# Optimization experiments

Measured on AMD Instinct MI355X. Metric: run time of the kernel, lower is better.

## Reference

```python
import jax, jax.numpy as jnp
import numpy as np

H = 64  # hidden size

def _lstm_forward(x, W_ih, W_hh, b_ih, b_hh):
    # x: [B, T, 1]; PyTorch gate order: i, f, g, o
    B = x.shape[0]
    # precompute input contribution for all timesteps: [B, T, 4H]
    x_gates = jnp.einsum('bti,gi->btg', x, W_ih) + b_ih + b_hh

    def step(carry, xg):
        h, c = carry                      # [B, H] each
        gates = xg + h @ W_hh.T           # [B, 4H]
        i = jax.nn.sigmoid(gates[:, 0*H:1*H])
        f = jax.nn.sigmoid(gates[:, 1*H:2*H])
        g = jnp.tanh(gates[:, 2*H:3*H])
        o = jax.nn.sigmoid(gates[:, 3*H:4*H])
        c_new = f * c + i * g
        h_new = o * jnp.tanh(c_new)
        return (h_new, c_new), None

    h0 = jnp.zeros((B, H), dtype=x.dtype)
    c0 = jnp.zeros((B, H), dtype=x.dtype)
    (h_last, _), _ = jax.lax.scan(step, (h0, c0), jnp.swapaxes(x_gates, 0, 1))
    return h_last

def setup_inputs() -> dict:
    key = jax.random.key(0)
    ks = jax.random.split(key, 7)
    B, T = 262144, 5
    s = 1.0 / np.sqrt(H)  # pytorch LSTM default init scale
    return {
        'x':    jax.random.normal(ks[0], (B, T, 1), dtype=jnp.float32),
        'W_ih': jax.random.uniform(ks[1], (4*H, 1), jnp.float32, -s, s),
        'W_hh': jax.random.uniform(ks[2], (4*H, H), jnp.float32, -s, s),
        'b_ih': jax.random.uniform(ks[3], (4*H,), jnp.float32, -s, s),
        'b_hh': jax.random.uniform(ks[4], (4*H,), jnp.float32, -s, s),
        'W_fc': jax.random.uniform(ks[5], (1, H), jnp.float32, -s, s),
        'b_fc': jax.random.uniform(ks[6], (1,), jnp.float32, -s, s),
    }

def reference(x, W_ih, W_hh, b_ih, b_hh, W_fc, b_fc):
    h_last = _lstm_forward(x, W_ih, W_hh, b_ih, b_hh)  # [B, H]
    return h_last @ W_fc.T + b_fc                      # [B, 1]
```

## Files before the change

### kernel.cpp

```cpp
#include <hip/hip_runtime.h>

#define HDIM   64
#define TSTEPS 5
#define WAVES  8
#define BLOCK  (WAVES * 64)
#define EPW    16
#define EPB    (WAVES * EPW)

typedef _Float16 f16x8 __attribute__((ext_vector_type(8)));
typedef float    f32x4 __attribute__((ext_vector_type(4)));

#define L2E 1.44269504088896340736f

__device__ __forceinline__ float rcp_(float x) { return __builtin_amdgcn_rcpf(x); }
__device__ __forceinline__ float ex2_(float x) { return __builtin_amdgcn_exp2f(x); }
__device__ __forceinline__ float sigp_(float v) { return rcp_(1.0f + ex2_(-v)); }

__global__ __launch_bounds__(BLOCK, 4) void lstm_mfma_kernel(
    const float* __restrict__ x,
    const float* __restrict__ W_ih,
    const float* __restrict__ W_hh,
    const float* __restrict__ b_ih,
    const float* __restrict__ b_hh,
    const float* __restrict__ W_fc,
    const float* __restrict__ b_fc,
    float* __restrict__ out,
    int B)
{
    __shared__ _Float16 Wf[2048 * 8];
    __shared__ _Float16 hbuf[WAVES * 1024];
    __shared__ float    wih_s[256];
    __shared__ float    cb_s[256];

    const int tid = threadIdx.x;

    #pragma unroll
    for (int s0 = 0; s0 < 2048; s0 += BLOCK) {
        const int s  = s0 + tid;
        const int ln = s & 63;
        const int kh = (s >> 6) & 1;
        const int n  = s >> 7;
        const float scl = ((n >> 2) == 2) ? (2.0f * L2E) : L2E;
        const int j  = n * 16 + (ln & 15);
        const int k0 = kh * 32 + ((ln >> 4) & 3) * 8;
        const float* src = W_hh + j * HDIM + k0;
        #pragma unroll
        for (int i = 0; i < 8; i++)
            Wf[s * 8 + i] = (_Float16)(src[i] * scl);
    }
    if (tid < 256) {
        const float scl = ((tid >> 6) == 2) ? (2.0f * L2E) : L2E;
        wih_s[tid] = W_ih[tid] * scl;
        cb_s[tid]  = (b_ih[tid] + b_hh[tid]) * scl;
    }
    __syncthreads();

    const int lane = tid & 63;
    const int wave = tid >> 6;
    const int m    = lane & 15;
    const int q    = lane >> 4;
    const int eg0  = (blockIdx.x * WAVES + wave) * EPW;

    _Float16* hb = hbuf + wave * 1024;

    const float* xp[4];
    #pragma unroll
    for (int r = 0; r < 4; r++) {
        int e = eg0 + q * 4 + r;
        if (e >= B) e = B - 1;
        xp[r] = x + (long)e * TSTEPS;
    }

    float c[16];
    float hv[16];

    for (int t = 0; t < TSTEPS; t++) {
        float xt[4];
        #pragma unroll
        for (int r = 0; r < 4; r++) xt[r] = xp[r][t];

        f16x8 hA0, hA1;
        if (t > 0) {
            hA0 = *(const f16x8*)(hb + lane * 8);
            hA1 = *(const f16x8*)(hb + 512 + lane * 8);
        }

        #pragma unroll
        for (int gr = 0; gr < 4; gr++) {
            float wihv[4], cbv[4];
            #pragma unroll
            for (int G = 0; G < 4; G++) {
                wihv[G] = wih_s[G * 64 + gr * 16 + m];
                cbv[G]  = cb_s[G * 64 + gr * 16 + m];
            }
            f32x4 ag[4];
            #pragma unroll
            for (int G = 0; G < 4; G++)
                #pragma unroll
                for (int r = 0; r < 4; r++)
                    ag[G][r] = fmaf(xt[r], wihv[G], cbv[G]);

            if (t > 0) {
                #pragma unroll
                for (int G = 0; G < 4; G++) {
                    const int n = G * 4 + gr;
                    f16x8 w0 = *(const f16x8*)(Wf + (n * 2 + 0) * 512 + lane * 8);
                    f16x8 w1 = *(const f16x8*)(Wf + (n * 2 + 1) * 512 + lane * 8);
                    ag[G] = __builtin_amdgcn_mfma_f32_16x16x32_f16(hA0, w0, ag[G], 0, 0, 0);
                    ag[G] = __builtin_amdgcn_mfma_f32_16x16x32_f16(hA1, w1, ag[G], 0, 0, 0);
                }
            }

            #pragma unroll
            for (int r = 0; r < 4; r++) {
                const int u = gr * 4 + r;
                const float si = sigp_(ag[0][r]);
                const float sf = sigp_(ag[1][r]);
                const float so = sigp_(ag[3][r]);
                const float rg  = rcp_(ex2_(ag[2][r]) + 1.0f);
                const float tgs = fmaf(rg, -4.0f * L2E, 2.0f * L2E);
                float cs = si * tgs;
                if (t > 0) cs = fmaf(sf, c[u], cs);
                c[u] = cs;
                const float rc = rcp_(ex2_(cs) + 1.0f);
                const float hn = so * fmaf(rc, -2.0f, 1.0f);
                hv[u] = hn;
                if (t < TSTEPS - 1) {
                    const int lp = (q * 4 + r) + 16 * (2 * (gr & 1) + (m >> 3));
                    hb[(gr >> 1) * 512 + lp * 8 + (m & 7)] = (_Float16)hn;
                }
            }
        }
    }

    float wfc[4];
    #pragma unroll
    for (int n = 0; n < 4; n++) wfc[n] = W_fc[n * 16 + m];
    const float bfc = b_fc[0];

    #pragma unroll
    for (int r = 0; r < 4; r++) {
        float p = hv[r] * wfc[0];
        p = fmaf(hv[4 + r],  wfc[1], p);
        p = fmaf(hv[8 + r],  wfc[2], p);
        p = fmaf(hv[12 + r], wfc[3], p);
        p += __shfl_xor(p, 1, 64);
        p += __shfl_xor(p, 2, 64);
        p += __shfl_xor(p, 4, 64);
        p += __shfl_xor(p, 8, 64);
        if (m == 0) {
            const int e = eg0 + q * 4 + r;
            if (e < B) out[e] = p + bfc;
        }
    }
}

extern "C" void kernel_launch(void* const* d_in, const int* in_sizes, int n_in,
                              void* d_out, int out_size, void* d_ws, size_t ws_size,
                              hipStream_t stream) {
    const float* x    = (const float*)d_in[0];
    const float* W_ih = (const float*)d_in[1];
    const float* W_hh = (const float*)d_in[2];
    const float* b_ih = (const float*)d_in[3];
    const float* b_hh = (const float*)d_in[4];
    const float* W_fc = (const float*)d_in[5];
    const float* b_fc = (const float*)d_in[6];
    float* out = (float*)d_out;

    const int B = in_sizes[0] / TSTEPS;
    const int grid = (B + EPB - 1) / EPB;
    lstm_mfma_kernel<<<grid, BLOCK, 0, stream>>>(x, W_ih, W_hh, b_ih, b_hh,
                                                 W_fc, b_fc, out, B);
}
```

Baseline: 153.7 us.

## Process two 16-row groups per wave, share W fragments, merge sigmoid reciprocals

Each wave now handles two independent 16-element batch groups. Every W_hh fragment loaded from LDS feeds MFMAs for both groups, which halves weight LDS traffic per element and interleaves two independent dependency chains. Gate activations share reciprocals by computing rcp of a product of two denominators, cutting transcendental ops. Input weights and biases are stored interleaved so each lane reads them as one vector. The final FC reads h back from LDS in MFMA layout and reduces with two shuffles instead of four. The cost is higher register pressure from holding two accumulator sets and two cell-state arrays, plus possible precision loss in the products of denominators.

```diff
diff --git a/kernel.cpp b/kernel.cpp
--- a/kernel.cpp
+++ b/kernel.cpp
@@ -4,7 +4,8 @@
 #define TSTEPS 5
 #define WAVES  8
 #define BLOCK  (WAVES * 64)
-#define EPW    16
+#define GPW    2
+#define EPW    (GPW * 16)
 #define EPB    (WAVES * EPW)
 
 typedef _Float16 f16x8 __attribute__((ext_vector_type(8)));
@@ -14,7 +15,6 @@
 
 __device__ __forceinline__ float rcp_(float x) { return __builtin_amdgcn_rcpf(x); }
 __device__ __forceinline__ float ex2_(float x) { return __builtin_amdgcn_exp2f(x); }
-__device__ __forceinline__ float sigp_(float v) { return rcp_(1.0f + ex2_(-v)); }
 
 __global__ __launch_bounds__(BLOCK, 4) void lstm_mfma_kernel(
     const float* __restrict__ x,
@@ -28,9 +28,9 @@
     int B)
 {
     __shared__ _Float16 Wf[2048 * 8];
-    __shared__ _Float16 hbuf[WAVES * 1024];
-    __shared__ float    wih_s[256];
-    __shared__ float    cb_s[256];
+    __shared__ _Float16 hbuf[WAVES * GPW * 1024];
+    __shared__ float    wih4[256];
+    __shared__ float    cb4[256];
 
     const int tid = threadIdx.x;
 
@@ -49,9 +49,10 @@
             Wf[s * 8 + i] = (_Float16)(src[i] * scl);
     }
     if (tid < 256) {
-        const float scl = ((tid >> 6) == 2) ? (2.0f * L2E) : L2E;
-        wih_s[tid] = W_ih[tid] * scl;
-        cb_s[tid]  = (b_ih[tid] + b_hh[tid]) * scl;
+        const int jl = tid >> 2, G = tid & 3;
+        const float scl = (G == 2) ? (2.0f * L2E) : L2E;
+        wih4[tid] = W_ih[G * 64 + jl] * scl;
+        cb4[tid]  = (b_ih[G * 64 + jl] + b_hh[G * 64 + jl]) * scl;
     }
     __syncthreads();
 
@@ -61,96 +62,130 @@
     const int q    = lane >> 4;
     const int eg0  = (blockIdx.x * WAVES + wave) * EPW;
 
-    _Float16* hb = hbuf + wave * 1024;
-
-    const float* xp[4];
-    #pragma unroll
-    for (int r = 0; r < 4; r++) {
-        int e = eg0 + q * 4 + r;
-        if (e >= B) e = B - 1;
-        xp[r] = x + (long)e * TSTEPS;
-    }
-
-    float c[16];
-    float hv[16];
-
+    _Float16* hb = hbuf + wave * (GPW * 1024);
+
+    int xo[GPW];
+    #pragma unroll
+    for (int g = 0; g < GPW; g++) {
+        int e4 = eg0 + g * 16 + q * 4;
+        if (e4 > B - 4) e4 = (B >= 4) ? (B - 4) : 0;
+        xo[g] = e4 * TSTEPS;
+    }
+
+    float c[GPW][16];
+
+    #pragma unroll
     for (int t = 0; t < TSTEPS; t++) {
-        float xt[4];
-        #pragma unroll
-        for (int r = 0; r < 4; r++) xt[r] = xp[r][t];
-
-        f16x8 hA0, hA1;
+        float xt[GPW][4];
+        #pragma unroll
+        for (int g = 0; g < GPW; g++)
+            #pragma unroll
+            for (int r = 0; r < 4; r++)
+                xt[g][r] = x[xo[g] + r * TSTEPS + t];
+
+        f16x8 hA[GPW][2];
         if (t > 0) {
-            hA0 = *(const f16x8*)(hb + lane * 8);
-            hA1 = *(const f16x8*)(hb + 512 + lane * 8);
+            #pragma unroll
+            for (int g = 0; g < GPW; g++) {
+                hA[g][0] = *(const f16x8*)(hb + g * 1024 + lane * 8);
+                hA[g][1] = *(const f16x8*)(hb + g * 1024 + 512 + lane * 8);
+            }
         }
 
         #pragma unroll
         for (int gr = 0; gr < 4; gr++) {
-            float wihv[4], cbv[4];
-            #pragma unroll
-            for (int G = 0; G < 4; G++) {
-                wihv[G] = wih_s[G * 64 + gr * 16 + m];
-                cbv[G]  = cb_s[G * 64 + gr * 16 + m];
-            }
-            f32x4 ag[4];
-            #pragma unroll
-            for (int G = 0; G < 4; G++)
+            const f32x4 wv  = *(const f32x4*)&wih4[(gr * 16 + m) * 4];
+            const f32x4 cbv = *(const f32x4*)&cb4[(gr * 16 + m) * 4];
+
+            f32x4 ag[GPW][4];
+            #pragma unroll
+            for (int g = 0; g < GPW; g++)
                 #pragma unroll
-                for (int r = 0; r < 4; r++)
-                    ag[G][r] = fmaf(xt[r], wihv[G], cbv[G]);
+                for (int G = 0; G < 4; G++)
+                    #pragma unroll
+                    for (int r = 0; r < 4; r++)
+                        ag[g][G][r] = fmaf(xt[g][r], wv[G], cbv[G]);
 
             if (t > 0) {
                 #pragma unroll
                 for (int G = 0; G < 4; G++) {
                     const int n = G * 4 + gr;
-                    f16x8 w0 = *(const f16x8*)(Wf + (n * 2 + 0) * 512 + lane * 8);
-                    f16x8 w1 = *(const f16x8*)(Wf + (n * 2 + 1) * 512 + lane * 8);
-                    ag[G] = __builtin_amdgcn_mfma_f32_16x16x32_f16(hA0, w0, ag[G], 0, 0, 0);
-                    ag[G] = __builtin_amdgcn_mfma_f32_16x16x32_f16(hA1, w1, ag[G], 0, 0, 0);
+                    const f16x8 w0 = *(const f16x8*)(Wf + (n * 2 + 0) * 512 + lane * 8);
+                    const f16x8 w1 = *(const f16x8*)(Wf + (n * 2 + 1) * 512 + lane * 8);
+                    #pragma unroll
+                    for (int g = 0; g < GPW; g++) {
+                        ag[g][G] = __builtin_amdgcn_mfma_f32_16x16x32_f16(hA[g][0], w0, ag[g][G], 0, 0, 0);
+                        ag[g][G] = __builtin_amdgcn_mfma_f32_16x16x32_f16(hA[g][1], w1, ag[g][G], 0, 0, 0);
+                    }
                 }
             }
 
             #pragma unroll
-            for (int r = 0; r < 4; r++) {
-                const int u = gr * 4 + r;
-                const float si = sigp_(ag[0][r]);
-                const float sf = sigp_(ag[1][r]);
-                const float so = sigp_(ag[3][r]);
-                const float rg  = rcp_(ex2_(ag[2][r]) + 1.0f);
-                const float tgs = fmaf(rg, -4.0f * L2E, 2.0f * L2E);
-                float cs = si * tgs;
-                if (t > 0) cs = fmaf(sf, c[u], cs);
-                c[u] = cs;
-                const float rc = rcp_(ex2_(cs) + 1.0f);
-                const float hn = so * fmaf(rc, -2.0f, 1.0f);
-                hv[u] = hn;
-                if (t < TSTEPS - 1) {
+            for (int g = 0; g < GPW; g++) {
+                #pragma unroll
+                for (int r = 0; r < 4; r++) {
+                    const int u = gr * 4 + r;
+                    float cs, so;
+                    if (t == 0) {
+                        const float ei = ex2_(-ag[g][0][r]);
+                        const float eg = ex2_( ag[g][2][r]);
+                        const float eo = ex2_(-ag[g][3][r]);
+                        const float si = rcp_(1.0f + ei);
+                        const float dg = 1.0f + eg, dn = 1.0f + eo;
+                        const float r2 = rcp_(dn * dg);
+                        so = r2 * dg;
+                        const float rg  = r2 * dn;
+                        const float tgs = fmaf(rg, -4.0f * L2E, 2.0f * L2E);
+                        cs = si * tgs;
+                    } else {
+                        const float ei = ex2_(-ag[g][0][r]);
+                        const float ef = ex2_(-ag[g][1][r]);
+                        const float eg = ex2_( ag[g][2][r]);
+                        const float eo = ex2_(-ag[g][3][r]);
+                        const float di = 1.0f + ei, df = 1.0f + ef;
+                        const float dg = 1.0f + eg, dn = 1.0f + eo;
+                        const float r1 = rcp_(di * df);
+                        const float si = r1 * df, sf = r1 * di;
+                        const float r2 = rcp_(dn * dg);
+                        so = r2 * dg;
+                        const float rg  = r2 * dn;
+                        const float tgs = fmaf(rg, -4.0f * L2E, 2.0f * L2E);
+                        cs = fmaf(sf, c[g][u], si * tgs);
+                    }
+                    c[g][u] = cs;
+                    const float rc = rcp_(ex2_(cs) + 1.0f);
+                    const float hn = so * fmaf(rc, -2.0f, 1.0f);
                     const int lp = (q * 4 + r) + 16 * (2 * (gr & 1) + (m >> 3));
-                    hb[(gr >> 1) * 512 + lp * 8 + (m & 7)] = (_Float16)hn;
+                    hb[g * 1024 + (gr >> 1) * 512 + lp * 8 + (m & 7)] = (_Float16)hn;
                 }
             }
         }
     }
 
-    float wfc[4];
-    #pragma unroll
-    for (int n = 0; n < 4; n++) wfc[n] = W_fc[n * 16 + m];
+    float p[GPW] = {0.0f, 0.0f};
+    #pragma unroll
+    for (int kh = 0; kh < 2; kh++) {
+        const float* wp = W_fc + kh * 32 + q * 8;
+        const f32x4 wa = *(const f32x4*)wp;
+        const f32x4 wb = *(const f32x4*)(wp + 4);
+        #pragma unroll
+        for (int g = 0; g < GPW; g++) {
+            const f16x8 h8 = *(const f16x8*)(hb + g * 1024 + kh * 512 + lane * 8);
+            #pragma unroll
+            for (int i = 0; i < 4; i++) {
+                p[g] = fmaf((float)h8[i],     wa[i], p[g]);
+                p[g] = fmaf((float)h8[4 + i], wb[i], p[g]);
+            }
+        }
+    }
     const float bfc = b_fc[0];
-
-    #pragma unroll
-    for (int r = 0; r < 4; r++) {
-        float p = hv[r] * wfc[0];
-        p = fmaf(hv[4 + r],  wfc[1], p);
-        p = fmaf(hv[8 + r],  wfc[2], p);
-        p = fmaf(hv[12 + r], wfc[3], p);
-        p += __shfl_xor(p, 1, 64);
-        p += __shfl_xor(p, 2, 64);
-        p += __shfl_xor(p, 4, 64);
-        p += __shfl_xor(p, 8, 64);
-        if (m == 0) {
-            const int e = eg0 + q * 4 + r;
-            if (e < B) out[e] = p + bfc;
+    #pragma unroll
+    for (int g = 0; g < GPW; g++) {
+        p[g] += __shfl_xor(p[g], 16, 64);
+        p[g] += __shfl_xor(p[g], 32, 64);
+        if (lane < 16) {
+            const int e = eg0 + g * 16 + lane;
+            if (e < B) out[e] = p[g] + bfc;
         }
     }
 }
```

Measured after the change: 188.8 us. 1.23x slower.
